# Kernel tuning notes

Hardware: AMD Instinct MI355X
Metric: run time of the kernel (lower is better)

Reference implementation:

```python
import jax, jax.numpy as jnp
import numpy as np

N = 100000   # nodes
E = 1600000  # edges
IN = 128     # in_dim
C = 32       # hidden_dim
H = 2        # heads1
G = 64       # graphs in batch
NEG_SLOPE = 0.2


def setup_inputs() -> dict:
    key = jax.random.key(0)
    ks = jax.random.split(key, 20)
    f = lambda k, shape: jax.random.normal(k, shape, dtype=jnp.float32) * 0.05
    return {
        "x": jax.random.normal(ks[0], (N, IN), dtype=jnp.float32),
        "edge_index": jax.random.randint(ks[1], (2, E), 0, N, dtype=jnp.int32),
        "batch": jnp.sort(jax.random.randint(ks[2], (N,), 0, G, dtype=jnp.int32)),
        # GATv2 layer 1: lin_l / lin_r [IN, H*C], att [H, C], bias [H*C]
        "Wl1": f(ks[3], (IN, H * C)), "Wr1": f(ks[4], (IN, H * C)),
        "att1": f(ks[5], (H, C)), "b1": f(ks[6], (H * C,)),
        # GATv2 layer 2: heads=1
        "Wl2": f(ks[7], (H * C, C)), "Wr2": f(ks[8], (H * C, C)),
        "att2": f(ks[9], (1, C)), "b2": f(ks[10], (C,)),
        # GlobalAttention gate_nn: Linear(C,C) -> ReLU -> Linear(C,1)
        "g1w": f(ks[11], (C, C)), "g1b": f(ks[12], (C,)),
        "g2w": f(ks[13], (C, 1)), "g2b": f(ks[14], (1,)),
        # MLP head
        "lin1w": f(ks[15], (C, C)), "lin1b": f(ks[16], (C,)),
        "lin2w": f(ks[17], (C, 1)), "lin2b": f(ks[18], (1,)),
    }


def _gatv2(x, src, dst, Wl, Wr, att, bias, heads, ch):
    """PyG GATv2Conv (concat=True, share_weights=False, eval mode)."""
    n = x.shape[0]
    xl = (x @ Wl).reshape(n, heads, ch)  # source transform (also the message)
    xr = (x @ Wr).reshape(n, heads, ch)  # target transform
    e = jax.nn.leaky_relu(xl[src] + xr[dst], negative_slope=NEG_SLOPE)  # [E,H,C]
    score = jnp.einsum('ehc,hc->eh', e, att)  # [E,H]
    # scatter-softmax over incoming edges of each destination node
    m = jax.ops.segment_max(score, dst, num_segments=n)
    m = jnp.where(jnp.isfinite(m), m, 0.0)  # nodes w/o in-edges
    ex = jnp.exp(score - m[dst])
    denom = jax.ops.segment_sum(ex, dst, num_segments=n)
    alpha = ex / denom[dst]  # [E,H]
    out = jax.ops.segment_sum(alpha[:, :, None] * xl[src], dst, num_segments=n)
    return out.reshape(n, heads * ch) + bias


def reference(x, edge_index, batch, Wl1, Wr1, att1, b1, Wl2, Wr2, att2, b2,
              g1w, g1b, g2w, g2b, lin1w, lin1b, lin2w, lin2b):
    src, dst = edge_index[0], edge_index[1]
    h = jax.nn.relu(_gatv2(x, src, dst, Wl1, Wr1, att1, b1, H, C))   # [N, H*C]
    h = jax.nn.relu(_gatv2(h, src, dst, Wl2, Wr2, att2, b2, 1, C))   # [N, C]
    # GlobalAttention pooling: softmax(gate_nn(h)) over nodes of each graph
    gate = jax.nn.relu(h @ g1w + g1b) @ g2w + g2b                     # [N,1]
    gm = jax.ops.segment_max(gate, batch, num_segments=G)
    gm = jnp.where(jnp.isfinite(gm), gm, 0.0)
    ge = jnp.exp(gate - gm[batch])
    gd = jax.ops.segment_sum(ge, batch, num_segments=G)
    attw = ge / gd[batch]                                             # [N,1]
    pooled = jax.ops.segment_sum(attw * h, batch, num_segments=G)     # [G,C]
    z = jax.nn.relu(pooled @ lin1w + lin1b)
    return (z @ lin2w + lin2b).squeeze(-1)                            # [G]
```

## Files before the change

kernel.cpp:

```cpp
#include <hip/hip_runtime.h>
#include <hip/hip_fp16.h>
#include <cfloat>
#include <cstdint>
#include <cstddef>

#define N_NODES 100000
#define N_EDGES 1600000
#define G_GRAPHS 64
#define BKT_SHIFT 9
#define BKT_NODES (1 << BKT_SHIFT)
#define NBKT ((N_NODES + BKT_NODES - 1) >> BKT_SHIFT)

typedef _Float16 hvec2 __attribute__((ext_vector_type(2)));
typedef _Float16 hvec4 __attribute__((ext_vector_type(4)));
typedef _Float16 hvec8 __attribute__((ext_vector_type(8)));
typedef float f32x4 __attribute__((ext_vector_type(4)));

static __device__ __forceinline__ float fdot2(hvec2 a, hvec2 b, float c) {
#if __has_builtin(__builtin_amdgcn_fdot2)
  return __builtin_amdgcn_fdot2(a, b, c, false);
#else
  return fmaf((float)a.y, (float)b.y, fmaf((float)a.x, (float)b.x, c));
#endif
}

static __device__ __forceinline__ hvec2 leaky2(hvec2 v) {
  return __builtin_elementwise_max(v, v * (_Float16)0.2f);
}

__launch_bounds__(256) __global__
void prepw_kernel(const float* __restrict__ Wl, const float* __restrict__ Wr,
                  __half* __restrict__ Wh, int K_, int J_) {
  const int idx = blockIdx.x * 256 + threadIdx.x;
  if (idx >= 2 * K_ * J_) return;
  const int j2 = idx / K_;
  const int k = idx - j2 * K_;
  const int j = (j2 < J_) ? j2 : j2 - J_;
  const float v = (j2 < J_) ? Wl[k * J_ + j] : Wr[k * J_ + j];
  Wh[idx] = __float2half(v);
}

template <int K, int J, bool FUSE>
__launch_bounds__(256) __global__
void gemm_mfma(const float* __restrict__ A, const __half* __restrict__ Wh,
               const float* __restrict__ bias, __half* __restrict__ O0,
               float* __restrict__ O1, int n) {
  constexpr int BM = 64;
  constexpr int KP = K + 8;
  constexpr int J2 = 2 * J;
  __shared__ __align__(16) __half Alds[BM][KP];
  __shared__ __align__(16) __half Wlds[J2][KP];
  const int tid = threadIdx.x;
  const int n0 = blockIdx.x * BM;

  for (int c = tid; c < J2 * (K / 8); c += 256) {
    const int j = c / (K / 8);
    const int k8 = c - j * (K / 8);
    const uint4 w = reinterpret_cast<const uint4*>(Wh)[c];
    *reinterpret_cast<uint4*>(&Wlds[j][k8 * 8]) = w;
  }
  for (int c = tid; c < BM * (K / 4); c += 256) {
    const int r = c / (K / 4);
    const int k4 = c - r * (K / 4);
    const int row = n0 + r;
    float4 v = make_float4(0.f, 0.f, 0.f, 0.f);
    if (row < n) {
      v = reinterpret_cast<const float4*>(A)[(size_t)row * (K / 4) + k4];
      if constexpr (FUSE) {
        const float4 b = reinterpret_cast<const float4*>(bias)[k4];
        v.x = fmaxf(v.x + b.x, 0.f);
        v.y = fmaxf(v.y + b.y, 0.f);
        v.z = fmaxf(v.z + b.z, 0.f);
        v.w = fmaxf(v.w + b.w, 0.f);
      }
    }
    const hvec4 h = {(_Float16)v.x, (_Float16)v.y, (_Float16)v.z,
                     (_Float16)v.w};
    *reinterpret_cast<hvec4*>(&Alds[r][k4 * 4]) = h;
  }
  __syncthreads();

  const int wv = tid >> 6;
  const int l = tid & 63;
  const int lr = l & 15;
  const int lk = l >> 4;

  hvec8 afrag[K / 32];
#pragma unroll
  for (int kc = 0; kc < K / 32; ++kc)
    afrag[kc] = *reinterpret_cast<const hvec8*>(
        &Alds[wv * 16 + lr][kc * 32 + 8 * lk]);

#pragma unroll
  for (int jt = 0; jt < J2 / 16; ++jt) {
    f32x4 acc = {0.f, 0.f, 0.f, 0.f};
#pragma unroll
    for (int kc = 0; kc < K / 32; ++kc) {
      const hvec8 b = *reinterpret_cast<const hvec8*>(
          &Wlds[jt * 16 + lr][kc * 32 + 8 * lk]);
      acc = __builtin_amdgcn_mfma_f32_16x16x32_f16(afrag[kc], b, acc, 0, 0, 0);
    }
    const int colt = jt * 16 + lr;
    const int rowb = n0 + wv * 16 + 4 * lk;
#pragma unroll
    for (int r = 0; r < 4; ++r) {
      const int row = rowb + r;
      if (row < n) {
        if constexpr (true) {
          if (jt < J / 16)
            O0[(size_t)row * J + colt] = __float2half(acc[r]);
          else
            O1[(size_t)row * J + (colt - J)] = acc[r];
        }
      }
    }
  }
}

__launch_bounds__(256) __global__
void histB_kernel(const int* __restrict__ ei, int* __restrict__ bhist) {
  __shared__ int lb[NBKT];
  for (int i = threadIdx.x; i < NBKT; i += 256) lb[i] = 0;
  __syncthreads();
  const int e0 = blockIdx.x * 1024 + threadIdx.x;
#pragma unroll
  for (int k = 0; k < 4; ++k) {
    const int e = e0 + k * 256;
    if (e < N_EDGES) atomicAdd(&lb[ei[N_EDGES + e] >> BKT_SHIFT], 1);
  }
  __syncthreads();
  for (int i = threadIdx.x; i < NBKT; i += 256)
    if (lb[i]) atomicAdd(&bhist[i], lb[i]);
}

__launch_bounds__(256) __global__
void bscan_kernel(const int* __restrict__ bhist, int* __restrict__ bbase,
                  int* __restrict__ bcursor) {
  __shared__ int ls[256];
  const int tid = threadIdx.x;
  const int v = (tid < NBKT) ? bhist[tid] : 0;
  ls[tid] = v;
  __syncthreads();
  for (int d = 1; d < 256; d <<= 1) {
    const int t = (tid >= d) ? ls[tid - d] : 0;
    __syncthreads();
    ls[tid] += t;
    __syncthreads();
  }
  if (tid < NBKT) {
    const int ex = ls[tid] - v;
    bbase[tid] = ex;
    bcursor[tid] = ex;
  }
}

__launch_bounds__(1024) __global__
void partA_kernel(const int* __restrict__ ei, int* __restrict__ bcursor,
                  int2* __restrict__ staging) {
  __shared__ int lh[NBKT];
  __shared__ int lbase[NBKT];
  const int tid = threadIdx.x;
  for (int i = tid; i < NBKT; i += 1024) lh[i] = 0;
  __syncthreads();
  const int e0 = blockIdx.x * 4096 + tid;
  int s[4], d[4];
#pragma unroll
  for (int k = 0; k < 4; ++k) {
    const int e = e0 + k * 1024;
    const bool ok = e < N_EDGES;
    s[k] = ok ? ei[e] : 0;
    d[k] = ok ? ei[N_EDGES + e] : -1;
    if (ok) atomicAdd(&lh[d[k] >> BKT_SHIFT], 1);
  }
  __syncthreads();
  for (int i = tid; i < NBKT; i += 1024) {
    const int c = lh[i];
    lbase[i] = c ? atomicAdd(&bcursor[i], c) : 0;
    lh[i] = 0;
  }
  __syncthreads();
#pragma unroll
  for (int k = 0; k < 4; ++k) {
    if (d[k] >= 0) {
      const int b = d[k] >> BKT_SHIFT;
      const int p = lbase[b] + atomicAdd(&lh[b], 1);
      staging[p] = make_int2(s[k], d[k]);
    }
  }
}

__launch_bounds__(256) __global__
void partB_kernel(const int2* __restrict__ staging,
                  const int* __restrict__ bbase, const int* __restrict__ bhist,
                  int2* __restrict__ rowdeg, int* __restrict__ csr_src) {
  __shared__ int ldeg[BKT_NODES];
  __shared__ int lsc[256];
  const int b = blockIdx.x;
  const int tid = threadIdx.x;
  const int node0 = b << BKT_SHIFT;
  ldeg[2 * tid] = 0;
  ldeg[2 * tid + 1] = 0;
  __syncthreads();
  const int start = bbase[b];
  const int cnt = bhist[b];
  for (int i = tid; i < cnt; i += 256)
    atomicAdd(&ldeg[staging[start + i].y - node0], 1);
  __syncthreads();
  const int d0 = ldeg[2 * tid];
  const int d1 = ldeg[2 * tid + 1];
  const int psum = d0 + d1;
  lsc[tid] = psum;
  __syncthreads();
  for (int d = 1; d < 256; d <<= 1) {
    const int t = (tid >= d) ? lsc[tid - d] : 0;
    __syncthreads();
    lsc[tid] += t;
    __syncthreads();
  }
  const int ex = lsc[tid] - psum + start;
  const int n0 = node0 + 2 * tid;
  if (n0 < N_NODES)
    *reinterpret_cast<int4*>(&rowdeg[n0]) = make_int4(ex, d0, ex + d0, d1);
  __syncthreads();
  ldeg[2 * tid] = ex;
  ldeg[2 * tid + 1] = ex + d0;
  __syncthreads();
  for (int i = tid; i < cnt; i += 256) {
    const int2 e = staging[start + i];
    const int p = atomicAdd(&ldeg[e.y - node0], 1);
    csr_src[p] = e.x;
  }
}

__launch_bounds__(256) __global__
void gat1_kernel(const __half* __restrict__ xlh, const float* __restrict__ xr,
                 const float* __restrict__ att, const int2* __restrict__ rowdeg,
                 const int* __restrict__ csr_src, float* __restrict__ agg) {
  const int n =
      __builtin_amdgcn_readfirstlane(blockIdx.x * 4 + (threadIdx.x >> 6));
  if (n >= N_NODES) return;
  const int lane = threadIdx.x & 63;
  const int g = lane >> 4;
  const int m = lane & 15;
  const int2 rd = rowdeg[n];
  const int r0 = __builtin_amdgcn_readfirstlane(rd.x);
  const int dg = __builtin_amdgcn_readfirstlane(rd.y);

  const float4 xrf =
      *reinterpret_cast<const float4*>(xr + ((size_t)n << 6) + 4 * m);
  const hvec2 xh01 = {(_Float16)xrf.x, (_Float16)xrf.y};
  const hvec2 xh23 = {(_Float16)xrf.z, (_Float16)xrf.w};
  const float4 atf = *reinterpret_cast<const float4*>(att + 4 * m);
  const hvec2 at01 = {(_Float16)atf.x, (_Float16)atf.y};
  const hvec2 at23 = {(_Float16)atf.z, (_Float16)atf.w};

  float s = 0.f, acc0 = 0.f, acc1 = 0.f, acc2 = 0.f, acc3 = 0.f;

  auto gather1 = [&](int q, int srcv) -> uint2 {
    const int sel = __shfl(srcv, 4 * q + g);
    return *reinterpret_cast<const uint2*>(
        (const char*)xlh + (((size_t)(unsigned)sel) << 7) + 8 * m);
  };
  auto compute1 = [&](int q, uint2 buf, int rem) {
    const hvec2 a01 = __builtin_bit_cast(hvec2, buf.x);
    const hvec2 a23 = __builtin_bit_cast(hvec2, buf.y);
    const hvec2 v01 = leaky2(a01 + xh01);
    const hvec2 v23 = leaky2(a23 + xh23);
    float p = fdot2(v23, at23, fdot2(v01, at01, 0.f));
    p += __shfl_xor(p, 1);
    p += __shfl_xor(p, 2);
    p += __shfl_xor(p, 4);
    float e = __expf(p);
    e = (4 * q + g < rem) ? e : 0.f;
    s += e;
    acc0 = fmaf(e, (float)a01.x, acc0);
    acc1 = fmaf(e, (float)a01.y, acc1);
    acc2 = fmaf(e, (float)a23.x, acc2);
    acc3 = fmaf(e, (float)a23.y, acc3);
  };

  for (int c0 = 0; c0 < dg; c0 += 64) {
    const int rem = dg - c0;
    int srcv = 0;
    if (lane < rem) srcv = csr_src[r0 + c0 + lane];
    const int Kc = (min(rem, 64) + 3) >> 2;
#pragma unroll
    for (int g0 = 0; g0 < 16; g0 += 4) {
      if (g0 < Kc) {
        uint2 B[4];
#pragma unroll
        for (int k = 0; k < 4; ++k)
          if (g0 + k < Kc) B[k] = gather1(g0 + k, srcv);
#pragma unroll
        for (int k = 0; k < 4; ++k)
          if (g0 + k < Kc) compute1(g0 + k, B[k], rem);
      }
    }
  }

  s += __shfl_xor(s, 16);
  s += __shfl_xor(s, 32);
  acc0 += __shfl_xor(acc0, 16);
  acc0 += __shfl_xor(acc0, 32);
  acc1 += __shfl_xor(acc1, 16);
  acc1 += __shfl_xor(acc1, 32);
  acc2 += __shfl_xor(acc2, 16);
  acc2 += __shfl_xor(acc2, 32);
  acc3 += __shfl_xor(acc3, 16);
  acc3 += __shfl_xor(acc3, 32);
  const float inv = s > 0.f ? 1.f / s : 0.f;
  if (g == 0)
    *reinterpret_cast<float4*>(agg + ((size_t)n << 6) + 4 * m) =
        make_float4(acc0 * inv, acc1 * inv, acc2 * inv, acc3 * inv);
}

__launch_bounds__(256) __global__
void gat2_kernel(const __half* __restrict__ xlh, const float* __restrict__ xr,
                 const float* __restrict__ att, const int2* __restrict__ rowdeg,
                 const int* __restrict__ csr_src,
                 const float* __restrict__ b2, const float* __restrict__ g1w,
                 const float* __restrict__ g1b, const float* __restrict__ g2w,
                 const float* __restrict__ g2b, float* __restrict__ h2,
                 float* __restrict__ gate) {
  const int n =
      __builtin_amdgcn_readfirstlane(blockIdx.x * 4 + (threadIdx.x >> 6));
  if (n >= N_NODES) return;
  const int lane = threadIdx.x & 63;
  const int g = lane >> 3;
  const int m = lane & 7;
  const int2 rd = rowdeg[n];
  const int r0 = __builtin_amdgcn_readfirstlane(rd.x);
  const int dg = __builtin_amdgcn_readfirstlane(rd.y);

  const float4 xrf =
      *reinterpret_cast<const float4*>(xr + (size_t)n * 32 + 4 * m);
  const hvec2 xh01 = {(_Float16)xrf.x, (_Float16)xrf.y};
  const hvec2 xh23 = {(_Float16)xrf.z, (_Float16)xrf.w};
  const float4 atf = *reinterpret_cast<const float4*>(att + 4 * m);
  const hvec2 at01 = {(_Float16)atf.x, (_Float16)atf.y};
  const hvec2 at23 = {(_Float16)atf.z, (_Float16)atf.w};

  float s = 0.f, acc0 = 0.f, acc1 = 0.f, acc2 = 0.f, acc3 = 0.f;

  auto gather1 = [&](int q, int srcv) -> uint2 {
    const int sel = __shfl(srcv, 8 * q + g);
    return *reinterpret_cast<const uint2*>(
        (const char*)xlh + (((size_t)(unsigned)sel) << 6) + 8 * m);
  };
  auto compute1 = [&](int q, uint2 buf, int rem) {
    const hvec2 a01 = __builtin_bit_cast(hvec2, buf.x);
    const hvec2 a23 = __builtin_bit_cast(hvec2, buf.y);
    const hvec2 v01 = leaky2(a01 + xh01);
    const hvec2 v23 = leaky2(a23 + xh23);
    float p = fdot2(v23, at23, fdot2(v01, at01, 0.f));
    p += __shfl_xor(p, 1);
    p += __shfl_xor(p, 2);
    p += __shfl_xor(p, 4);
    float e = __expf(p);
    e = (8 * q + g < rem) ? e : 0.f;
    s += e;
    acc0 = fmaf(e, (float)a01.x, acc0);
    acc1 = fmaf(e, (float)a01.y, acc1);
    acc2 = fmaf(e, (float)a23.x, acc2);
    acc3 = fmaf(e, (float)a23.y, acc3);
  };

  for (int c0 = 0; c0 < dg; c0 += 64) {
    const int rem = dg - c0;
    int srcv = 0;
    if (lane < rem) srcv = csr_src[r0 + c0 + lane];
    const int Kc = (min(rem, 64) + 7) >> 3;
#pragma unroll
    for (int g0 = 0; g0 < 8; g0 += 4) {
      if (g0 < Kc) {
        uint2 B[4];
#pragma unroll
        for (int k = 0; k < 4; ++k)
          if (g0 + k < Kc) B[k] = gather1(g0 + k, srcv);
#pragma unroll
        for (int k = 0; k < 4; ++k)
          if (g0 + k < Kc) compute1(g0 + k, B[k], rem);
      }
    }
  }

  s += __shfl_xor(s, 8);
  s += __shfl_xor(s, 16);
  s += __shfl_xor(s, 32);
  acc0 += __shfl_xor(acc0, 8);
  acc0 += __shfl_xor(acc0, 16);
  acc0 += __shfl_xor(acc0, 32);
  acc1 += __shfl_xor(acc1, 8);
  acc1 += __shfl_xor(acc1, 16);
  acc1 += __shfl_xor(acc1, 32);
  acc2 += __shfl_xor(acc2, 8);
  acc2 += __shfl_xor(acc2, 16);
  acc2 += __shfl_xor(acc2, 32);
  acc3 += __shfl_xor(acc3, 8);
  acc3 += __shfl_xor(acc3, 16);
  acc3 += __shfl_xor(acc3, 32);
  const float inv = s > 0.f ? 1.f / s : 0.f;
  const float4 b2v = *reinterpret_cast<const float4*>(b2 + 4 * m);
  const float h0 = fmaxf(fmaf(acc0, inv, b2v.x), 0.f);
  const float h1 = fmaxf(fmaf(acc1, inv, b2v.y), 0.f);
  const float h2v = fmaxf(fmaf(acc2, inv, b2v.z), 0.f);
  const float h3 = fmaxf(fmaf(acc3, inv, b2v.w), 0.f);
  if (g == 0)
    *reinterpret_cast<float4*>(h2 + (size_t)n * 32 + 4 * m) =
        make_float4(h0, h1, h2v, h3);

  const int c = lane & 31;
  const float t0 = __shfl(h0, c >> 2, 8);
  const float t1 = __shfl(h1, c >> 2, 8);
  const float t2 = __shfl(h2v, c >> 2, 8);
  const float t3 = __shfl(h3, c >> 2, 8);
  const float hv = (c & 2) ? ((c & 1) ? t3 : t2) : ((c & 1) ? t1 : t0);
  const int k0 = (lane >> 5) << 4;
  float sg = 0.f;
#pragma unroll
  for (int k = 0; k < 16; ++k) {
    const int kk = k0 + k;
    sg = fmaf(__shfl(hv, kk, 32), g1w[kk * 32 + c], sg);
  }
  sg += __shfl_xor(sg, 32);
  sg = fmaxf(sg + g1b[c], 0.f);
  float pg = sg * g2w[c];
  pg += __shfl_xor(pg, 1);
  pg += __shfl_xor(pg, 2);
  pg += __shfl_xor(pg, 4);
  pg += __shfl_xor(pg, 8);
  pg += __shfl_xor(pg, 16);
  if (lane == 0) gate[n] = pg + g2b[0];
}

__launch_bounds__(256) __global__
void gepool_kernel(const float* __restrict__ h2, const int* __restrict__ batch,
                   const float* __restrict__ gate, float* __restrict__ gd,
                   float* __restrict__ pooled) {
  __shared__ float pool[G_GRAPHS * 32];
  __shared__ float gdb[G_GRAPHS];
  const int tid = threadIdx.x;
  for (int i = tid; i < G_GRAPHS * 32; i += 256) pool[i] = 0.f;
  if (tid < G_GRAPHS) gdb[tid] = 0.f;
  __syncthreads();
  const int c = tid & 31;
  const int hw = tid >> 5;
  const int start = blockIdx.x * 256;
  const int end = min(N_NODES, start + 256);
  for (int n = start + hw; n < end; n += 8) {
    const int b = batch[n];
    const float ge = __expf(gate[n]);
    atomicAdd(&pool[b * 32 + c], ge * h2[(size_t)n * 32 + c]);
    if (c == 0) atomicAdd(&gdb[b], ge);
  }
  __syncthreads();
  for (int i = tid; i < G_GRAPHS * 32; i += 256)
    if (pool[i] != 0.f) unsafeAtomicAdd(&pooled[i], pool[i]);
  if (tid < G_GRAPHS && gdb[tid] != 0.f) unsafeAtomicAdd(&gd[tid], gdb[tid]);
}

__launch_bounds__(64) __global__
void final_kernel(const float* __restrict__ pooled, const float* __restrict__ gd,
                  const float* __restrict__ l1w, const float* __restrict__ l1b,
                  const float* __restrict__ l2w, const float* __restrict__ l2b,
                  float* __restrict__ out) {
  const int g = blockIdx.x;
  const int lane = threadIdx.x;
  if (lane >= 32) return;
  const float invgd = 1.f / gd[g];
  float s = l1b[lane];
#pragma unroll
  for (int k = 0; k < 32; ++k)
    s = fmaf(pooled[g * 32 + k] * invgd, l1w[k * 32 + lane], s);
  s = fmaxf(s, 0.f);
  float p = s * l2w[lane];
  p += __shfl_xor(p, 1);
  p += __shfl_xor(p, 2);
  p += __shfl_xor(p, 4);
  p += __shfl_xor(p, 8);
  p += __shfl_xor(p, 16);
  if (lane == 0) out[g] = p + l2b[0];
}

extern "C" void kernel_launch(void* const* d_in, const int* in_sizes, int n_in,
                              void* d_out, int out_size, void* d_ws,
                              size_t ws_size, hipStream_t stream) {
  const float* x    = (const float*)d_in[0];
  const int*   ei   = (const int*)d_in[1];
  const int*   batch= (const int*)d_in[2];
  const float* Wl1  = (const float*)d_in[3];
  const float* Wr1  = (const float*)d_in[4];
  const float* att1 = (const float*)d_in[5];
  const float* b1   = (const float*)d_in[6];
  const float* Wl2  = (const float*)d_in[7];
  const float* Wr2  = (const float*)d_in[8];
  const float* att2 = (const float*)d_in[9];
  const float* b2   = (const float*)d_in[10];
  const float* g1w  = (const float*)d_in[11];
  const float* g1b  = (const float*)d_in[12];
  const float* g2w  = (const float*)d_in[13];
  const float* g2b  = (const float*)d_in[14];
  const float* l1w  = (const float*)d_in[15];
  const float* l1b  = (const float*)d_in[16];
  const float* l2w  = (const float*)d_in[17];
  const float* l2b  = (const float*)d_in[18];
  float* out = (float*)d_out;

  int* bhist   = (int*)d_ws;
  int* bbase   = bhist + NBKT;
  int* bcursor = bbase + NBKT;
  int2* rowdeg = (int2*)(bcursor + NBKT);
  int* csr_src = (int*)(rowdeg + N_NODES);
  int2* staging = (int2*)(csr_src + N_EDGES + 16);
  float* fbase = (float*)(staging + N_EDGES);
  float* xr1  = fbase;
  float* agg1 = xr1 + (size_t)N_NODES * 64;
  float* gate = agg1 + (size_t)N_NODES * 64;
  float* gd   = gate + N_NODES;
  float* pooled = gd + G_GRAPHS;
  __half* xl1h = (__half*)(pooled + G_GRAPHS * 32);
  __half* xl2h = xl1h;
  float* xr2 = xr1;
  float* h2  = xr1 + (size_t)N_NODES * 32;
  __half* Wh1 = (__half*)gate;
  __half* Wh2 = Wh1 + 128 * 128;

  (void)hipMemsetAsync(bhist, 0, (size_t)NBKT * sizeof(int), stream);
  (void)hipMemsetAsync(gd, 0,
                       (size_t)(G_GRAPHS + G_GRAPHS * 32) * sizeof(float),
                       stream);

  prepw_kernel<<<(2 * 128 * 64 + 255) / 256, 256, 0, stream>>>(Wl1, Wr1, Wh1,
                                                               128, 64);
  prepw_kernel<<<(2 * 64 * 32 + 255) / 256, 256, 0, stream>>>(Wl2, Wr2, Wh2,
                                                              64, 32);

  histB_kernel<<<(N_EDGES + 1023) / 1024, 256, 0, stream>>>(ei, bhist);
  bscan_kernel<<<1, 256, 0, stream>>>(bhist, bbase, bcursor);
  partA_kernel<<<(N_EDGES + 4095) / 4096, 1024, 0, stream>>>(ei, bcursor,
                                                             staging);
  partB_kernel<<<NBKT, 256, 0, stream>>>(staging, bbase, bhist, rowdeg,
                                         csr_src);

  gemm_mfma<128, 64, false><<<(N_NODES + 63) / 64, 256, 0, stream>>>(
      x, Wh1, nullptr, xl1h, xr1, N_NODES);
  gat1_kernel<<<(N_NODES + 3) / 4, 256, 0, stream>>>(xl1h, xr1, att1, rowdeg,
                                                     csr_src, agg1);

  gemm_mfma<64, 32, true><<<(N_NODES + 63) / 64, 256, 0, stream>>>(
      agg1, Wh2, b1, xl2h, xr2, N_NODES);
  gat2_kernel<<<(N_NODES + 3) / 4, 256, 0, stream>>>(
      xl2h, xr2, att2, rowdeg, csr_src, b2, g1w, g1b, g2w, g2b, h2, gate);

  gepool_kernel<<<(N_NODES + 255) / 256, 256, 0, stream>>>(h2, batch, gate, gd,
                                                           pooled);
  final_kernel<<<64, 64, 0, stream>>>(pooled, gd, l1w, l1b, l2w, l2b, out);
}
```

Measured before the change: 373.8 us.

## Use DPP reductions, exp2 scoring, direct CSR loads, split gate MLP into own kernel

The GAT edge loops now use DPP lane adds instead of shuffles for the 8-lane score reduction. Attention weights are prescaled by log2(e) so the hardware exp2 can be used directly. Each lane loads its source index straight from CSR instead of broadcasting through shuffles, with the CSR array padded and zeroed so reads past the end stay safe. The gate MLP moves out of gat2 into a separate kernel that stages the weights in LDS, which adds a launch and another pass over h2.

```diff
diff --git a/kernel.cpp b/kernel.cpp
--- a/kernel.cpp
+++ b/kernel.cpp
@@ -10,11 +10,14 @@
 #define BKT_SHIFT 9
 #define BKT_NODES (1 << BKT_SHIFT)
 #define NBKT ((N_NODES + BKT_NODES - 1) >> BKT_SHIFT)
+#define CSR_PAD 80
 
 typedef _Float16 hvec2 __attribute__((ext_vector_type(2)));
 typedef _Float16 hvec4 __attribute__((ext_vector_type(4)));
 typedef _Float16 hvec8 __attribute__((ext_vector_type(8)));
 typedef float f32x4 __attribute__((ext_vector_type(4)));
+
+#define LOG2E 1.4426950408889634f
 
 static __device__ __forceinline__ float fdot2(hvec2 a, hvec2 b, float c) {
 #if __has_builtin(__builtin_amdgcn_fdot2)
@@ -26,6 +29,27 @@
 
 static __device__ __forceinline__ hvec2 leaky2(hvec2 v) {
   return __builtin_elementwise_max(v, v * (_Float16)0.2f);
+}
+
+static __device__ __forceinline__ float fast_exp2(float x) {
+#if __has_builtin(__builtin_amdgcn_exp2f)
+  return __builtin_amdgcn_exp2f(x);
+#else
+  return exp2f(x);
+#endif
+}
+
+template <int CTRL>
+static __device__ __forceinline__ float dppadd(float v) {
+  const int vi = __builtin_bit_cast(int, v);
+  const int ti = __builtin_amdgcn_update_dpp(0, vi, CTRL, 0xF, 0xF, true);
+  return v + __builtin_bit_cast(float, ti);
+}
+static __device__ __forceinline__ float dpp_sum8(float v) {
+  v = dppadd<0xB1>(v);
+  v = dppadd<0x4E>(v);
+  v = dppadd<0x141>(v);
+  return v;
 }
 
 __launch_bounds__(256) __global__
@@ -106,12 +130,10 @@
     for (int r = 0; r < 4; ++r) {
       const int row = rowb + r;
       if (row < n) {
-        if constexpr (true) {
-          if (jt < J / 16)
-            O0[(size_t)row * J + colt] = __float2half(acc[r]);
-          else
-            O1[(size_t)row * J + (colt - J)] = acc[r];
-        }
+        if (jt < J / 16)
+          O0[(size_t)row * J + colt] = __float2half(acc[r]);
+        else
+          O1[(size_t)row * J + (colt - J)] = acc[r];
       }
     }
   }
@@ -198,6 +220,7 @@
   const int b = blockIdx.x;
   const int tid = threadIdx.x;
   const int node0 = b << BKT_SHIFT;
+  if (b == 0 && tid < CSR_PAD) csr_src[N_EDGES + tid] = 0;
   ldeg[2 * tid] = 0;
   ldeg[2 * tid + 1] = 0;
   __syncthreads();
@@ -251,13 +274,12 @@
   const hvec2 xh01 = {(_Float16)xrf.x, (_Float16)xrf.y};
   const hvec2 xh23 = {(_Float16)xrf.z, (_Float16)xrf.w};
   const float4 atf = *reinterpret_cast<const float4*>(att + 4 * m);
-  const hvec2 at01 = {(_Float16)atf.x, (_Float16)atf.y};
-  const hvec2 at23 = {(_Float16)atf.z, (_Float16)atf.w};
+  const hvec2 at01 = {(_Float16)(atf.x * LOG2E), (_Float16)(atf.y * LOG2E)};
+  const hvec2 at23 = {(_Float16)(atf.z * LOG2E), (_Float16)(atf.w * LOG2E)};
 
   float s = 0.f, acc0 = 0.f, acc1 = 0.f, acc2 = 0.f, acc3 = 0.f;
 
-  auto gather1 = [&](int q, int srcv) -> uint2 {
-    const int sel = __shfl(srcv, 4 * q + g);
+  auto gather1 = [&](int sel) -> uint2 {
     return *reinterpret_cast<const uint2*>(
         (const char*)xlh + (((size_t)(unsigned)sel) << 7) + 8 * m);
   };
@@ -267,10 +289,8 @@
     const hvec2 v01 = leaky2(a01 + xh01);
     const hvec2 v23 = leaky2(a23 + xh23);
     float p = fdot2(v23, at23, fdot2(v01, at01, 0.f));
-    p += __shfl_xor(p, 1);
-    p += __shfl_xor(p, 2);
-    p += __shfl_xor(p, 4);
-    float e = __expf(p);
+    p = dpp_sum8(p);
+    float e = fast_exp2(p);
     e = (4 * q + g < rem) ? e : 0.f;
     s += e;
     acc0 = fmaf(e, (float)a01.x, acc0);
@@ -281,16 +301,18 @@
 
   for (int c0 = 0; c0 < dg; c0 += 64) {
     const int rem = dg - c0;
-    int srcv = 0;
-    if (lane < rem) srcv = csr_src[r0 + c0 + lane];
+    const int* cp = csr_src + r0 + c0 + (lane >> 4);
     const int Kc = (min(rem, 64) + 3) >> 2;
 #pragma unroll
     for (int g0 = 0; g0 < 16; g0 += 4) {
       if (g0 < Kc) {
+        int sq[4];
+#pragma unroll
+        for (int k = 0; k < 4; ++k) sq[k] = cp[4 * (g0 + k)];
         uint2 B[4];
 #pragma unroll
         for (int k = 0; k < 4; ++k)
-          if (g0 + k < Kc) B[k] = gather1(g0 + k, srcv);
+          if (g0 + k < Kc) B[k] = gather1(sq[k]);
 #pragma unroll
         for (int k = 0; k < 4; ++k)
           if (g0 + k < Kc) compute1(g0 + k, B[k], rem);
@@ -317,11 +339,8 @@
 __launch_bounds__(256) __global__
 void gat2_kernel(const __half* __restrict__ xlh, const float* __restrict__ xr,
                  const float* __restrict__ att, const int2* __restrict__ rowdeg,
-                 const int* __restrict__ csr_src,
-                 const float* __restrict__ b2, const float* __restrict__ g1w,
-                 const float* __restrict__ g1b, const float* __restrict__ g2w,
-                 const float* __restrict__ g2b, float* __restrict__ h2,
-                 float* __restrict__ gate) {
+                 const int* __restrict__ csr_src, const float* __restrict__ b2,
+                 float* __restrict__ h2) {
   const int n =
       __builtin_amdgcn_readfirstlane(blockIdx.x * 4 + (threadIdx.x >> 6));
   if (n >= N_NODES) return;
@@ -337,13 +356,12 @@
   const hvec2 xh01 = {(_Float16)xrf.x, (_Float16)xrf.y};
   const hvec2 xh23 = {(_Float16)xrf.z, (_Float16)xrf.w};
   const float4 atf = *reinterpret_cast<const float4*>(att + 4 * m);
-  const hvec2 at01 = {(_Float16)atf.x, (_Float16)atf.y};
-  const hvec2 at23 = {(_Float16)atf.z, (_Float16)atf.w};
+  const hvec2 at01 = {(_Float16)(atf.x * LOG2E), (_Float16)(atf.y * LOG2E)};
+  const hvec2 at23 = {(_Float16)(atf.z * LOG2E), (_Float16)(atf.w * LOG2E)};
 
   float s = 0.f, acc0 = 0.f, acc1 = 0.f, acc2 = 0.f, acc3 = 0.f;
 
-  auto gather1 = [&](int q, int srcv) -> uint2 {
-    const int sel = __shfl(srcv, 8 * q + g);
+  auto gather1 = [&](int sel) -> uint2 {
     return *reinterpret_cast<const uint2*>(
         (const char*)xlh + (((size_t)(unsigned)sel) << 6) + 8 * m);
   };
@@ -353,10 +371,8 @@
     const hvec2 v01 = leaky2(a01 + xh01);
     const hvec2 v23 = leaky2(a23 + xh23);
     float p = fdot2(v23, at23, fdot2(v01, at01, 0.f));
-    p += __shfl_xor(p, 1);
-    p += __shfl_xor(p, 2);
-    p += __shfl_xor(p, 4);
-    float e = __expf(p);
+    p = dpp_sum8(p);
+    float e = fast_exp2(p);
     e = (8 * q + g < rem) ? e : 0.f;
     s += e;
     acc0 = fmaf(e, (float)a01.x, acc0);
@@ -367,16 +383,18 @@
 
   for (int c0 = 0; c0 < dg; c0 += 64) {
     const int rem = dg - c0;
-    int srcv = 0;
-    if (lane < rem) srcv = csr_src[r0 + c0 + lane];
+    const int* cp = csr_src + r0 + c0 + (lane >> 3);
     const int Kc = (min(rem, 64) + 7) >> 3;
 #pragma unroll
     for (int g0 = 0; g0 < 8; g0 += 4) {
       if (g0 < Kc) {
+        int sq[4];
+#pragma unroll
+        for (int k = 0; k < 4; ++k) sq[k] = cp[8 * (g0 + k)];
         uint2 B[4];
 #pragma unroll
         for (int k = 0; k < 4; ++k)
-          if (g0 + k < Kc) B[k] = gather1(g0 + k, srcv);
+          if (g0 + k < Kc) B[k] = gather1(sq[k]);
 #pragma unroll
         for (int k = 0; k < 4; ++k)
           if (g0 + k < Kc) compute1(g0 + k, B[k], rem);
@@ -401,36 +419,44 @@
   acc3 += __shfl_xor(acc3, 32);
   const float inv = s > 0.f ? 1.f / s : 0.f;
   const float4 b2v = *reinterpret_cast<const float4*>(b2 + 4 * m);
-  const float h0 = fmaxf(fmaf(acc0, inv, b2v.x), 0.f);
-  const float h1 = fmaxf(fmaf(acc1, inv, b2v.y), 0.f);
-  const float h2v = fmaxf(fmaf(acc2, inv, b2v.z), 0.f);
-  const float h3 = fmaxf(fmaf(acc3, inv, b2v.w), 0.f);
   if (g == 0)
     *reinterpret_cast<float4*>(h2 + (size_t)n * 32 + 4 * m) =
-        make_float4(h0, h1, h2v, h3);
-
-  const int c = lane & 31;
-  const float t0 = __shfl(h0, c >> 2, 8);
-  const float t1 = __shfl(h1, c >> 2, 8);
-  const float t2 = __shfl(h2v, c >> 2, 8);
-  const float t3 = __shfl(h3, c >> 2, 8);
-  const float hv = (c & 2) ? ((c & 1) ? t3 : t2) : ((c & 1) ? t1 : t0);
-  const int k0 = (lane >> 5) << 4;
-  float sg = 0.f;
-#pragma unroll
-  for (int k = 0; k < 16; ++k) {
-    const int kk = k0 + k;
-    sg = fmaf(__shfl(hv, kk, 32), g1w[kk * 32 + c], sg);
-  }
-  sg += __shfl_xor(sg, 32);
-  sg = fmaxf(sg + g1b[c], 0.f);
+        make_float4(fmaxf(fmaf(acc0, inv, b2v.x), 0.f),
+                    fmaxf(fmaf(acc1, inv, b2v.y), 0.f),
+                    fmaxf(fmaf(acc2, inv, b2v.z), 0.f),
+                    fmaxf(fmaf(acc3, inv, b2v.w), 0.f));
+}
+
+__launch_bounds__(256) __global__
+void gate_kernel(const float* __restrict__ h2, const float* __restrict__ g1w,
+                 const float* __restrict__ g1b, const float* __restrict__ g2w,
+                 const float* __restrict__ g2b, float* __restrict__ gate) {
+  __shared__ float Wg[32 * 32];
+  __shared__ float Hs[8][32];
+  const int tid = threadIdx.x;
+  for (int i = tid; i < 1024; i += 256) Wg[i] = g1w[i];
+  const int c = tid & 31;
+  const int slot = tid >> 5;
+  const int n = blockIdx.x * 8 + slot;
+  Hs[slot][c] = (n < N_NODES) ? h2[(size_t)n * 32 + c] : 0.f;
+  __syncthreads();
+  float sg = g1b[c];
+#pragma unroll
+  for (int k4 = 0; k4 < 8; ++k4) {
+    const float4 hq = *reinterpret_cast<const float4*>(&Hs[slot][4 * k4]);
+    sg = fmaf(hq.x, Wg[(4 * k4 + 0) * 32 + c], sg);
+    sg = fmaf(hq.y, Wg[(4 * k4 + 1) * 32 + c], sg);
+    sg = fmaf(hq.z, Wg[(4 * k4 + 2) * 32 + c], sg);
+    sg = fmaf(hq.w, Wg[(4 * k4 + 3) * 32 + c], sg);
+  }
+  sg = fmaxf(sg, 0.f);
   float pg = sg * g2w[c];
   pg += __shfl_xor(pg, 1);
   pg += __shfl_xor(pg, 2);
   pg += __shfl_xor(pg, 4);
   pg += __shfl_xor(pg, 8);
   pg += __shfl_xor(pg, 16);
-  if (lane == 0) gate[n] = pg + g2b[0];
+  if (c == 0 && n < N_NODES) gate[n] = pg + g2b[0];
 }
 
 __launch_bounds__(256) __global__
@@ -511,7 +537,7 @@
   int* bcursor = bbase + NBKT;
   int2* rowdeg = (int2*)(bcursor + NBKT);
   int* csr_src = (int*)(rowdeg + N_NODES);
-  int2* staging = (int2*)(csr_src + N_EDGES + 16);
+  int2* staging = (int2*)(csr_src + N_EDGES + CSR_PAD);
   float* fbase = (float*)(staging + N_EDGES);
   float* xr1  = fbase;
   float* agg1 = xr1 + (size_t)N_NODES * 64;
@@ -549,8 +575,10 @@
 
   gemm_mfma<64, 32, true><<<(N_NODES + 63) / 64, 256, 0, stream>>>(
       agg1, Wh2, b1, xl2h, xr2, N_NODES);
-  gat2_kernel<<<(N_NODES + 3) / 4, 256, 0, stream>>>(
-      xl2h, xr2, att2, rowdeg, csr_src, b2, g1w, g1b, g2w, g2b, h2, gate);
+  gat2_kernel<<<(N_NODES + 3) / 4, 256, 0, stream>>>(xl2h, xr2, att2, rowdeg,
+                                                     csr_src, b2, h2);
+  gate_kernel<<<(N_NODES + 7) / 8, 256, 0, stream>>>(h2, g1w, g1b, g2w, g2b,
+                                                     gate);
 
   gepool_kernel<<<(N_NODES + 255) / 256, 256, 0, stream>>>(h2, batch, gate, gd,
                                                            pooled);
```

Result: no change. 380.1 us (+1.7%).
